# Kernel tuning notes

Hardware: AMD Instinct MI355X
Metric: run time of the kernel (lower is better)

Reference implementation:

```python
import jax, jax.numpy as jnp
import numpy as np

EPS = 1e-07
N = 524288      # samples (columns x layers)
C = 42          # n_channel
NC = 8          # n_constituent
HID = [5, 4, 4] # hidden widths per MLP
OUT = 3         # absorbed / transmitted / reflected split


def _make_mlp_params(key, n_in):
    """Stacked per-channel MLP params: weights [C,out,in], biases [C,out]."""
    dims = [n_in] + HID + [OUT]
    Ws, bs = [], []
    for i in range(len(dims) - 1):
        key, kw, kb = jax.random.split(key, 3)
        W = jax.random.uniform(kw, (C, dims[i + 1], dims[i]), minval=-1.0, maxval=1.0)
        if i < len(dims) - 2:  # hidden bias ~ U(0.9, 1.1)
            b = jax.random.uniform(kb, (C, dims[i + 1]), minval=0.9, maxval=1.1)
        else:                  # output bias ~ U(-0.1, 0.1)
            b = jax.random.uniform(kb, (C, dims[i + 1]), minval=-0.1, maxval=0.1)
        Ws.append(W)
        bs.append(b)
    return Ws, bs


def setup_inputs() -> dict:
    key = jax.random.key(0)
    k0, k1, k2, k3, kd, kf = jax.random.split(key, 6)
    inp = {
        "tau": jax.random.uniform(k0, (N, C, NC), dtype=jnp.float32) * 0.5,
        "mu_direct": jax.random.uniform(k1, (N, 1), minval=0.05, maxval=1.0, dtype=jnp.float32),
        "mu_diffuse": jax.random.uniform(k2, (N, 1), minval=0.05, maxval=1.0, dtype=jnp.float32),
        "constituents": jax.random.uniform(k3, (N, NC), dtype=jnp.float32),
    }
    Wd, bd = _make_mlp_params(kd, NC + 1)  # direct nets take mu appended
    Wf, bf = _make_mlp_params(kf, NC)      # diffuse nets
    for i in range(4):
        inp[f"Wd{i}"], inp[f"bd{i}"] = Wd[i], bd[i]
        inp[f"Wf{i}"], inp[f"bf{i}"] = Wf[i], bf[i]
    return inp


def _batched_mlp_softmax(x, Ws, bs):
    # x: [N, n_in] shared across channels; Ws[i]: [C, out, in]; bs[i]: [C, out]
    h = jnp.einsum('ni,coi->nco', x, Ws[0]) + bs[0]
    h = jax.nn.relu(h)
    for W, b in zip(Ws[1:-1], bs[1:-1]):
        h = jax.nn.relu(jnp.einsum('nci,coi->nco', h, W) + b)
    logits = jnp.einsum('nci,coi->nco', h, Ws[-1]) + bs[-1]  # [N, C, 3]
    return jax.nn.softmax(logits, axis=-1)


def reference(tau, mu_direct, mu_diffuse, constituents,
              Wd0, bd0, Wd1, bd1, Wd2, bd2, Wd3, bd3,
              Wf0, bf0, Wf1, bf1, Wf2, bf2, Wf3, bf3):
    tau_total = jnp.sum(tau, axis=2)                    # [N, C]
    t_direct = jnp.exp(-tau_total / (mu_direct + EPS))  # mu [N,1] broadcasts over C
    t_diffuse = jnp.exp(-tau_total / (mu_diffuse + EPS))

    cons_direct = jnp.concatenate(
        [constituents / (mu_direct + EPS), mu_direct], axis=1)  # [N, NC+1]

    e_split_direct = _batched_mlp_softmax(
        cons_direct, [Wd0, Wd1, Wd2, Wd3], [bd0, bd1, bd2, bd3])   # [N, C, 3]
    e_split_diffuse = _batched_mlp_softmax(
        constituents, [Wf0, Wf1, Wf2, Wf3], [bf0, bf1, bf2, bf3])  # [N, C, 3]

    return (t_direct, t_diffuse, e_split_direct, e_split_diffuse)
```

## Files before the change

### kernel.cpp

```cpp
#include <hip/hip_runtime.h>

#define EPS 1e-7f
#define CCH 42
#define NCON 8

typedef float v4f __attribute__((ext_vector_type(4)));
typedef float v2f __attribute__((ext_vector_type(2)));

template<int NIN>
__device__ __forceinline__ void mlp_softmax3(
    const float x[NIN], int c,
    const float* __restrict__ W0, const float* __restrict__ b0,
    const float* __restrict__ W1, const float* __restrict__ b1,
    const float* __restrict__ W2, const float* __restrict__ b2,
    const float* __restrict__ W3, const float* __restrict__ b3,
    float o[3])
{
    float h0[5];
#pragma unroll
    for (int j = 0; j < 5; ++j) {
        const float* w = W0 + (c * 5 + j) * NIN;
        float a = b0[c * 5 + j];
#pragma unroll
        for (int i = 0; i < NIN; ++i) a = fmaf(x[i], w[i], a);
        h0[j] = fmaxf(a, 0.0f);
    }
    float h1[4];
#pragma unroll
    for (int j = 0; j < 4; ++j) {
        const float* w = W1 + (c * 4 + j) * 5;
        float a = b1[c * 4 + j];
#pragma unroll
        for (int i = 0; i < 5; ++i) a = fmaf(h0[i], w[i], a);
        h1[j] = fmaxf(a, 0.0f);
    }
    float h2[4];
#pragma unroll
    for (int j = 0; j < 4; ++j) {
        const float* w = W2 + (c * 4 + j) * 4;
        float a = b2[c * 4 + j];
#pragma unroll
        for (int i = 0; i < 4; ++i) a = fmaf(h1[i], w[i], a);
        h2[j] = fmaxf(a, 0.0f);
    }
    float lg[3];
#pragma unroll
    for (int j = 0; j < 3; ++j) {
        const float* w = W3 + (c * 3 + j) * 4;
        float a = b3[c * 3 + j];
#pragma unroll
        for (int i = 0; i < 4; ++i) a = fmaf(h2[i], w[i], a);
        lg[j] = a;
    }
    float m = fmaxf(fmaxf(lg[0], lg[1]), lg[2]);
    float e0 = __expf(lg[0] - m);
    float e1 = __expf(lg[1] - m);
    float e2 = __expf(lg[2] - m);
    float r = __fdividef(1.0f, e0 + e1 + e2);
    o[0] = e0 * r;
    o[1] = e1 * r;
    o[2] = e2 * r;
}

__device__ __forceinline__ void phase_c(
    const v4f ta[4], const v4f tb[4],
    const float* __restrict__ mu_direct, const float* __restrict__ mu_diffuse,
    float* __restrict__ out, size_t nctot, int base_e, int per, int tid)
{
#pragma unroll
    for (int it = 0; it < 4; ++it) {
        int off = it * 384 + tid;
        if (off < per) {
            int e = base_e + off;
            v4f a = ta[it];
            v4f b = tb[it];
            float s = ((a.x + a.y) + (a.z + a.w)) + ((b.x + b.y) + (b.z + b.w));
            int nn = e / CCH;
            float md = mu_direct[nn] + EPS;
            float mf = mu_diffuse[nn] + EPS;
            __builtin_nontemporal_store(__expf(__fdividef(-s, md)), out + e);
            __builtin_nontemporal_store(__expf(__fdividef(-s, mf)), out + nctot + e);
        }
    }
}

__global__ __launch_bounds__(384, 6) void k_fused(
    const float* __restrict__ tau,
    const float* __restrict__ mu_direct,
    const float* __restrict__ mu_diffuse,
    const float* __restrict__ cons,
    const float* __restrict__ Wd0, const float* __restrict__ bd0,
    const float* __restrict__ Wf0, const float* __restrict__ bf0,
    const float* __restrict__ Wd1, const float* __restrict__ bd1,
    const float* __restrict__ Wf1, const float* __restrict__ bf1,
    const float* __restrict__ Wd2, const float* __restrict__ bd2,
    const float* __restrict__ Wf2, const float* __restrict__ bf2,
    const float* __restrict__ Wd3, const float* __restrict__ bd3,
    const float* __restrict__ Wf3, const float* __restrict__ bf3,
    float* __restrict__ out, int N)
{
    __shared__ float es[64 * 127];
    const int tid  = threadIdx.x;
    const int lane = tid & 63;
    const int wave = tid >> 6;
    const int n0   = blockIdx.x * 64;
    const int n    = n0 + lane;
    const bool direct = (blockIdx.y == 0);
    const size_t nctot = (size_t)N * CCH;

    float4 c0 = *(const float4*)(cons + (size_t)n * NCON);
    float4 c1 = *(const float4*)(cons + (size_t)n * NCON + 4);
    float mu  = direct ? mu_direct[n] : 0.0f;
    __builtin_amdgcn_sched_barrier(0);

    const int nblk = gridDim.x * 2;
    const int cid  = blockIdx.y * gridDim.x + blockIdx.x;
    const int per  = (int)(nctot / nblk);
    const int base_e = cid * per;
    v4f ta[4], tb[4];
#pragma unroll
    for (int it = 0; it < 4; ++it) {
        int off = it * 384 + tid;
        if (off < per) {
            const v4f* t4 = (const v4f*)tau + ((size_t)base_e + off) * 2;
            ta[it] = t4[0];
            tb[it] = t4[1];
        }
    }
    __builtin_amdgcn_sched_barrier(0);

    float x[9] = {c0.x, c0.y, c0.z, c0.w, c1.x, c1.y, c1.z, c1.w, 0.0f};
    if (direct) {
        float inv = __fdividef(1.0f, mu + EPS);
#pragma unroll
        for (int i = 0; i < 8; ++i) x[i] *= inv;
        x[8] = mu;
#pragma unroll 1
        for (int ci = 0; ci < 7; ++ci) {
            int c = __builtin_amdgcn_readfirstlane(wave * 7 + ci);
            float o[3];
            mlp_softmax3<9>(x, c, Wd0, bd0, Wd1, bd1, Wd2, bd2, Wd3, bd3, o);
#pragma unroll
            for (int k = 0; k < 3; ++k) es[lane * 127 + c * 3 + k] = o[k];
        }
    } else {
#pragma unroll 1
        for (int ci = 0; ci < 7; ++ci) {
            int c = __builtin_amdgcn_readfirstlane(wave * 7 + ci);
            float o[3];
            mlp_softmax3<8>(x, c, Wf0, bf0, Wf1, bf1, Wf2, bf2, Wf3, bf3, o);
#pragma unroll
            for (int k = 0; k < 3; ++k) es[lane * 127 + c * 3 + k] = o[k];
        }
    }
    __syncthreads();

    float* base = out + (direct ? 2 : 5) * nctot + (size_t)n0 * (CCH * 3);
    for (int idx = tid; idx < 64 * 63; idx += 384) {
        int r = idx / 63;
        int q = idx - r * 63;
        v2f v;
        v.x = es[r * 127 + 2 * q];
        v.y = es[r * 127 + 2 * q + 1];
        __builtin_nontemporal_store(v, (v2f*)base + idx);
    }

    phase_c(ta, tb, mu_direct, mu_diffuse, out, nctot, base_e, per, tid);
}

extern "C" void kernel_launch(void* const* d_in, const int* in_sizes, int n_in,
                              void* d_out, int out_size, void* d_ws, size_t ws_size,
                              hipStream_t stream) {
    const float* tau  = (const float*)d_in[0];
    const float* mud  = (const float*)d_in[1];
    const float* muf  = (const float*)d_in[2];
    const float* cons = (const float*)d_in[3];
    const float* Wd0 = (const float*)d_in[4];  const float* bd0 = (const float*)d_in[5];
    const float* Wf0 = (const float*)d_in[6];  const float* bf0 = (const float*)d_in[7];
    const float* Wd1 = (const float*)d_in[8];  const float* bd1 = (const float*)d_in[9];
    const float* Wf1 = (const float*)d_in[10]; const float* bf1 = (const float*)d_in[11];
    const float* Wd2 = (const float*)d_in[12]; const float* bd2 = (const float*)d_in[13];
    const float* Wf2 = (const float*)d_in[14]; const float* bf2 = (const float*)d_in[15];
    const float* Wd3 = (const float*)d_in[16]; const float* bd3 = (const float*)d_in[17];
    const float* Wf3 = (const float*)d_in[18]; const float* bf3 = (const float*)d_in[19];
    float* out = (float*)d_out;

    int N = in_sizes[1];
    dim3 grid(N / 64, 2);
    k_fused<<<grid, 384, 0, stream>>>(tau, mud, muf, cons,
                                      Wd0, bd0, Wf0, bf0,
                                      Wd1, bd1, Wf1, bf1,
                                      Wd2, bd2, Wf2, bf2,
                                      Wd3, bd3, Wf3, bf3,
                                      out, N);
}
```

Measured before the change: 293.1 us.

## Process direct and diffuse MLPs in one block and align tau work per sample

Each block now computes both the direct and the diffuse MLP for its 64 samples, so the grid's second dimension goes away and the constituents are loaded only once. The tau reduction work is remapped so that each block handles exactly the 64×42 channel elements of its own samples. This lets the mu values come from cross-lane shuffles instead of per-element global gathers. The tau loads are split into two stages so they overlap with the diffuse MLP and the shared-memory writeout. In exchange, each block does serial work with extra barriers, and it has fewer blocks and more registers in flight.

```diff
diff --git a/kernel.cpp b/kernel.cpp
--- a/kernel.cpp
+++ b/kernel.cpp
@@ -60,28 +60,6 @@
     o[0] = e0 * r;
     o[1] = e1 * r;
     o[2] = e2 * r;
-}
-
-__device__ __forceinline__ void phase_c(
-    const v4f ta[4], const v4f tb[4],
-    const float* __restrict__ mu_direct, const float* __restrict__ mu_diffuse,
-    float* __restrict__ out, size_t nctot, int base_e, int per, int tid)
-{
-#pragma unroll
-    for (int it = 0; it < 4; ++it) {
-        int off = it * 384 + tid;
-        if (off < per) {
-            int e = base_e + off;
-            v4f a = ta[it];
-            v4f b = tb[it];
-            float s = ((a.x + a.y) + (a.z + a.w)) + ((b.x + b.y) + (b.z + b.w));
-            int nn = e / CCH;
-            float md = mu_direct[nn] + EPS;
-            float mf = mu_diffuse[nn] + EPS;
-            __builtin_nontemporal_store(__expf(__fdividef(-s, md)), out + e);
-            __builtin_nontemporal_store(__expf(__fdividef(-s, mf)), out + nctot + e);
-        }
-    }
 }
 
 __global__ __launch_bounds__(384, 6) void k_fused(
@@ -105,67 +83,115 @@
     const int wave = tid >> 6;
     const int n0   = blockIdx.x * 64;
     const int n    = n0 + lane;
-    const bool direct = (blockIdx.y == 0);
     const size_t nctot = (size_t)N * CCH;
+    const int base_e = n0 * CCH;
 
     float4 c0 = *(const float4*)(cons + (size_t)n * NCON);
     float4 c1 = *(const float4*)(cons + (size_t)n * NCON + 4);
-    float mu  = direct ? mu_direct[n] : 0.0f;
+    float mud_own = mu_direct[n];
+    float muf_own = mu_diffuse[n];
     __builtin_amdgcn_sched_barrier(0);
 
-    const int nblk = gridDim.x * 2;
-    const int cid  = blockIdx.y * gridDim.x + blockIdx.x;
-    const int per  = (int)(nctot / nblk);
-    const int base_e = cid * per;
     v4f ta[4], tb[4];
 #pragma unroll
     for (int it = 0; it < 4; ++it) {
         int off = it * 384 + tid;
-        if (off < per) {
-            const v4f* t4 = (const v4f*)tau + ((size_t)base_e + off) * 2;
-            ta[it] = t4[0];
-            tb[it] = t4[1];
-        }
+        const v4f* t4 = (const v4f*)tau + ((size_t)base_e + off) * 2;
+        ta[it] = t4[0];
+        tb[it] = t4[1];
     }
     __builtin_amdgcn_sched_barrier(0);
 
-    float x[9] = {c0.x, c0.y, c0.z, c0.w, c1.x, c1.y, c1.z, c1.w, 0.0f};
-    if (direct) {
-        float inv = __fdividef(1.0f, mu + EPS);
-#pragma unroll
-        for (int i = 0; i < 8; ++i) x[i] *= inv;
-        x[8] = mu;
+    float xf[8] = {c0.x, c0.y, c0.z, c0.w, c1.x, c1.y, c1.z, c1.w};
+    {
+        float inv = __fdividef(1.0f, mud_own + EPS);
+        float xd[9];
+#pragma unroll
+        for (int i = 0; i < 8; ++i) xd[i] = xf[i] * inv;
+        xd[8] = mud_own;
 #pragma unroll 1
         for (int ci = 0; ci < 7; ++ci) {
             int c = __builtin_amdgcn_readfirstlane(wave * 7 + ci);
             float o[3];
-            mlp_softmax3<9>(x, c, Wd0, bd0, Wd1, bd1, Wd2, bd2, Wd3, bd3, o);
+            mlp_softmax3<9>(xd, c, Wd0, bd0, Wd1, bd1, Wd2, bd2, Wd3, bd3, o);
 #pragma unroll
             for (int k = 0; k < 3; ++k) es[lane * 127 + c * 3 + k] = o[k];
         }
-    } else {
+    }
+    __syncthreads();
+
+    {
+        float* base = out + 2 * nctot + (size_t)n0 * (CCH * 3);
+        for (int idx = tid; idx < 64 * 63; idx += 384) {
+            int r = idx / 63;
+            int q = idx - r * 63;
+            v2f v;
+            v.x = es[r * 127 + 2 * q];
+            v.y = es[r * 127 + 2 * q + 1];
+            __builtin_nontemporal_store(v, (v2f*)base + idx);
+        }
+    }
+    __syncthreads();
+
 #pragma unroll 1
-        for (int ci = 0; ci < 7; ++ci) {
-            int c = __builtin_amdgcn_readfirstlane(wave * 7 + ci);
-            float o[3];
-            mlp_softmax3<8>(x, c, Wf0, bf0, Wf1, bf1, Wf2, bf2, Wf3, bf3, o);
-#pragma unroll
-            for (int k = 0; k < 3; ++k) es[lane * 127 + c * 3 + k] = o[k];
+    for (int ci = 0; ci < 7; ++ci) {
+        int c = __builtin_amdgcn_readfirstlane(wave * 7 + ci);
+        float o[3];
+        mlp_softmax3<8>(xf, c, Wf0, bf0, Wf1, bf1, Wf2, bf2, Wf3, bf3, o);
+#pragma unroll
+        for (int k = 0; k < 3; ++k) es[lane * 127 + c * 3 + k] = o[k];
+    }
+
+#pragma unroll
+    for (int it = 0; it < 4; ++it) {
+        int off = it * 384 + tid;
+        int e = base_e + off;
+        v4f a = ta[it];
+        v4f b = tb[it];
+        float s = ((a.x + a.y) + (a.z + a.w)) + ((b.x + b.y) + (b.z + b.w));
+        int nnl = off / CCH;
+        float md = __shfl(mud_own, nnl) + EPS;
+        float mf = __shfl(muf_own, nnl) + EPS;
+        __builtin_nontemporal_store(__expf(__fdividef(-s, md)), out + e);
+        __builtin_nontemporal_store(__expf(__fdividef(-s, mf)), out + nctot + e);
+    }
+
+    v4f ta2[3], tb2[3];
+#pragma unroll
+    for (int j = 0; j < 3; ++j) {
+        int off = (4 + j) * 384 + tid;
+        const v4f* t4 = (const v4f*)tau + ((size_t)base_e + off) * 2;
+        ta2[j] = t4[0];
+        tb2[j] = t4[1];
+    }
+    __builtin_amdgcn_sched_barrier(0);
+    __syncthreads();
+
+    {
+        float* base = out + 5 * nctot + (size_t)n0 * (CCH * 3);
+        for (int idx = tid; idx < 64 * 63; idx += 384) {
+            int r = idx / 63;
+            int q = idx - r * 63;
+            v2f v;
+            v.x = es[r * 127 + 2 * q];
+            v.y = es[r * 127 + 2 * q + 1];
+            __builtin_nontemporal_store(v, (v2f*)base + idx);
         }
     }
-    __syncthreads();
-
-    float* base = out + (direct ? 2 : 5) * nctot + (size_t)n0 * (CCH * 3);
-    for (int idx = tid; idx < 64 * 63; idx += 384) {
-        int r = idx / 63;
-        int q = idx - r * 63;
-        v2f v;
-        v.x = es[r * 127 + 2 * q];
-        v.y = es[r * 127 + 2 * q + 1];
-        __builtin_nontemporal_store(v, (v2f*)base + idx);
-    }
-
-    phase_c(ta, tb, mu_direct, mu_diffuse, out, nctot, base_e, per, tid);
+
+#pragma unroll
+    for (int j = 0; j < 3; ++j) {
+        int off = (4 + j) * 384 + tid;
+        int e = base_e + off;
+        v4f a = ta2[j];
+        v4f b = tb2[j];
+        float s = ((a.x + a.y) + (a.z + a.w)) + ((b.x + b.y) + (b.z + b.w));
+        int nnl = off / CCH;
+        float md = __shfl(mud_own, nnl) + EPS;
+        float mf = __shfl(muf_own, nnl) + EPS;
+        __builtin_nontemporal_store(__expf(__fdividef(-s, md)), out + e);
+        __builtin_nontemporal_store(__expf(__fdividef(-s, mf)), out + nctot + e);
+    }
 }
 
 extern "C" void kernel_launch(void* const* d_in, const int* in_sizes, int n_in,
@@ -186,11 +212,10 @@
     float* out = (float*)d_out;
 
     int N = in_sizes[1];
-    dim3 grid(N / 64, 2);
-    k_fused<<<grid, 384, 0, stream>>>(tau, mud, muf, cons,
-                                      Wd0, bd0, Wf0, bf0,
-                                      Wd1, bd1, Wf1, bf1,
-                                      Wd2, bd2, Wf2, bf2,
-                                      Wd3, bd3, Wf3, bf3,
-                                      out, N);
+    k_fused<<<N / 64, 384, 0, stream>>>(tau, mud, muf, cons,
+                                        Wd0, bd0, Wf0, bf0,
+                                        Wd1, bd1, Wf1, bf1,
+                                        Wd2, bd2, Wf2, bf2,
+                                        Wd3, bd3, Wf3, bf3,
+                                        out, N);
 }
```

Measured after the change: 300.8 us. 2.6% more time.
